# Optimization experiments

Hardware: AMD Instinct MI355X
Metric: run time of the kernel (lower is better)

Reference implementation:

```python
import jax, jax.numpy as jnp
import numpy as np
from jax import lax

V, H, B, S, N, E = 32000, 128, 8, 512, 50000, 600000


def lstm(x, W_ih, W_hh, b):
    # x: [B,T,D]; W_ih: [4H,D]; W_hh: [4H,H]; b: [4H] (b_ih+b_hh combined)
    Bsz = x.shape[0]
    Hd = W_hh.shape[1]
    xg = jnp.einsum('btd,gd->btg', x, W_ih) + b  # precompute input gates [B,T,4H]
    h0 = jnp.zeros((Bsz, Hd), x.dtype)
    c0 = jnp.zeros((Bsz, Hd), x.dtype)

    def step(carry, g_t):
        h, c = carry
        g = g_t + h @ W_hh.T
        i, f, gg, o = jnp.split(g, 4, axis=-1)
        i = jax.nn.sigmoid(i)
        f = jax.nn.sigmoid(f)
        gg = jnp.tanh(gg)
        o = jax.nn.sigmoid(o)
        c = f * c + i * gg
        h = o * jnp.tanh(c)
        return (h, c), h

    _, hs = lax.scan(step, (h0, c0), jnp.swapaxes(xg, 0, 1))
    return jnp.swapaxes(hs, 0, 1)  # [B,T,H]


def gcn_conv(x, W, b, src, dst, n_nodes):
    # PyG GCNConv: add self-loops, symmetric normalization, out = A_hat (x W) + b
    h = x @ W.T  # [N,H]
    deg = jax.ops.segment_sum(jnp.ones(src.shape[0], x.dtype), dst, num_segments=n_nodes) + 1.0
    dinv = lax.rsqrt(deg)
    norm = dinv[src] * dinv[dst]  # [E]
    agg = jax.ops.segment_sum(h[src] * norm[:, None], dst, num_segments=n_nodes)
    agg = agg + h * (dinv * dinv)[:, None]  # self-loop contribution
    return agg + b


def setup_inputs() -> dict:
    key = jax.random.key(0)
    ks = jax.random.split(key, 20)
    s = 0.02
    return {
        'json_input': jax.random.randint(ks[0], (B, S), 0, V, dtype=jnp.int32),
        'node_ids': jax.random.randint(ks[1], (N,), 0, V, dtype=jnp.int32),
        'edge_index': jax.random.randint(ks[2], (2, E), 0, N, dtype=jnp.int32),
        'embedding': jax.random.normal(ks[3], (V, H), jnp.float32) * s,
        'W_ih_enc': jax.random.normal(ks[4], (4 * H, H), jnp.float32) * s,
        'W_hh_enc': jax.random.normal(ks[5], (4 * H, H), jnp.float32) * s,
        'b_enc': jnp.zeros((4 * H,), jnp.float32),
        'W1': jax.random.normal(ks[6], (H, H), jnp.float32) * s,
        'b1': jnp.zeros((H,), jnp.float32),
        'W2': jax.random.normal(ks[7], (H, H), jnp.float32) * s,
        'b2': jnp.zeros((H,), jnp.float32),
        'Wf': jax.random.normal(ks[8], (H, 2 * H), jnp.float32) * s,
        'bf': jnp.zeros((H,), jnp.float32),
        'W_ih_dec': jax.random.normal(ks[9], (4 * H, H), jnp.float32) * s,
        'W_hh_dec': jax.random.normal(ks[10], (4 * H, H), jnp.float32) * s,
        'b_dec': jnp.zeros((4 * H,), jnp.float32),
        'Wo': jax.random.normal(ks[11], (V, H), jnp.float32) * s,
        'bo': jnp.zeros((V,), jnp.float32),
    }


def reference(json_input, node_ids, edge_index, embedding, W_ih_enc, W_hh_enc, b_enc,
              W1, b1, W2, b2, Wf, bf, W_ih_dec, W_hh_dec, b_dec, Wo, bo):
    src, dst = edge_index[0], edge_index[1]
    # sequence branch
    json_emb = embedding[json_input]                      # [B,S,H]
    json_encoded = lstm(json_emb, W_ih_enc, W_hh_enc, b_enc)  # [B,S,H]
    # graph branch
    node_x = embedding[node_ids]                          # [N,H]
    x = gcn_conv(node_x, W1, b1, src, dst, node_ids.shape[0])
    x = gcn_conv(x, W2, b2, src, dst, node_ids.shape[0])
    # fusion
    graph_summary = jnp.broadcast_to(x.mean(axis=0, keepdims=True), (json_encoded.shape[0], x.shape[1]))
    combined = jnp.concatenate([json_encoded.mean(axis=1), graph_summary], axis=1)  # [B,2H]
    fused = combined @ Wf.T + bf                          # [B,H]
    fused_seq = jnp.broadcast_to(fused[:, None, :], (fused.shape[0], json_input.shape[1], fused.shape[1]))
    # decode
    decoded = lstm(fused_seq, W_ih_dec, W_hh_dec, b_dec)  # [B,S,H]
    return decoded @ Wo.T + bo                            # [B,S,V]
```

## Files before the change

### kernel.cpp

```cpp
#include <hip/hip_runtime.h>
#include <hip/hip_bf16.h>
#include <stdint.h>

#define VV 32000
#define HH 128
#define BB 8
#define SS 512
#define NNODE 50000
#define NEDGE 600000
#define NWORK 240

typedef __attribute__((ext_vector_type(8))) short s16x8;
typedef __attribute__((ext_vector_type(4))) float f32x4;

__device__ __forceinline__ void workers_barrier(int* bar, int tid) {
  __syncthreads();
  if (tid == 0) {
    int g = __hip_atomic_load(&bar[32], __ATOMIC_ACQUIRE, __HIP_MEMORY_SCOPE_AGENT);
    int old = __hip_atomic_fetch_add(&bar[0], 1, __ATOMIC_ACQ_REL, __HIP_MEMORY_SCOPE_AGENT);
    if (old == NWORK-1) {
      __hip_atomic_store(&bar[0], 0, __ATOMIC_RELAXED, __HIP_MEMORY_SCOPE_AGENT);
      __hip_atomic_store(&bar[32], g+1, __ATOMIC_RELEASE, __HIP_MEMORY_SCOPE_AGENT);
    } else {
      while (__hip_atomic_load(&bar[32], __ATOMIC_ACQUIRE, __HIP_MEMORY_SCOPE_AGENT) == g)
        __builtin_amdgcn_s_sleep(32);
    }
  }
  __syncthreads();
}

__global__ __launch_bounds__(512) void front_kernel(
    const int* __restrict__ jin, const float* __restrict__ emb,
    const float* __restrict__ WihE, const float* __restrict__ bE,
    float* xg, const float* __restrict__ WhhE, float* __restrict__ hmean,
    const float* __restrict__ Wo, __hip_bfloat16* __restrict__ Bhi, __hip_bfloat16* __restrict__ Blo,
    const int* __restrict__ esrc, const int* __restrict__ edst, const int* __restrict__ nids,
    float* __restrict__ deg, float* __restrict__ dinv, float* __restrict__ s1,
    float* __restrict__ s2, float* __restrict__ cc, float* __restrict__ ee,
    float* __restrict__ csum, float* __restrict__ gvec,
    const float* __restrict__ W1, const float* __restrict__ b1,
    const float* __restrict__ W2, const float* __restrict__ b2, float* __restrict__ mvec,
    int* ucnt, int* bar)
{
  __shared__ __align__(16) char shraw[131072];
  const int bid = blockIdx.x, tid = threadIdx.x;

  if (bid < 8) {
    float* h_s   = (float*)shraw;
    float* act_s = ((float*)shraw) + 128;
    const int b = bid;

    const f32x4* Wrow = (const f32x4*)(WhhE + (size_t)tid*HH);
    f32x4 w[32];
    #pragma unroll
    for (int k=0;k<32;k++) w[k] = Wrow[k];
    #pragma unroll
    for (int k=0;k<32;k++) asm volatile("" : "+v"(w[k]));

    const float* xgrow = xg + (size_t)b*SS*512;
    if (tid == 0) {
      while (__hip_atomic_load(&ucnt[(b*8+0)*32], __ATOMIC_ACQUIRE, __HIP_MEMORY_SCOPE_AGENT) < 8)
        __builtin_amdgcn_s_sleep(16);
    }
    __syncthreads();
    float xv = xgrow[tid];
    if (tid < 128) h_s[tid] = 0.f;
    float cstate = 0.f, hsum = 0.f;
    __syncthreads();

    for (int t=0;t<SS;t++) {
      if ((t & 63) == 0) {
        int cn = (t >> 6) + 1; if (cn > 7) cn = 7;
        if (tid == 0) {
          while (__hip_atomic_load(&ucnt[(b*8+cn)*32], __ATOMIC_ACQUIRE, __HIP_MEMORY_SCOPE_AGENT) < 8)
            __builtin_amdgcn_s_sleep(16);
        }
        __syncthreads();
      }
      int tn = (t < SS-1) ? (t+1) : t;
      float nxv = xgrow[(size_t)tn*512 + tid];
      float a0=0.f,a1=0.f,a2=0.f,a3=0.f;
      #pragma unroll
      for (int k=0;k<32;k++) {
        f32x4 hv = *(const f32x4*)&h_s[k*4];
        a0 += w[k].x*hv.x; a1 += w[k].y*hv.y;
        a2 += w[k].z*hv.z; a3 += w[k].w*hv.w;
      }
      float s = (a0+a1)+(a2+a3) + xv;
      int gid = tid >> 7;
      float act = (gid==2) ? tanhf(s) : 1.0f/(1.0f+expf(-s));
      act_s[tid] = act;
      __syncthreads();
      if (tid < 128) {
        float i_ = act_s[tid], f_ = act_s[128+tid], g_ = act_s[256+tid], o_ = act_s[384+tid];
        cstate = f_*cstate + i_*g_;
        float hh = o_*tanhf(cstate);
        h_s[tid] = hh;
        hsum += hh;
      }
      xv = nxv;
      __syncthreads();
    }
    if (tid < 128) hmean[b*HH + tid] = hsum * (1.0f/512.0f);
  } else {
    const int wbid = bid - 8;
    float (*arow)[128] = (float(*)[128])shraw;
    float* red = (float*)(shraw + 8*128*4);

    for (int u = wbid; u < 512; u += NWORK) {
      int c = u >> 6, r2 = u & 63, b = r2 >> 3, sub = r2 & 7;
      int row0 = b*512 + c*64 + sub*8;
      if (tid < 256) {
        int r = tid >> 5, c4 = (tid & 31) << 2;
        int tok = jin[row0 + r];
        *(float4*)&arow[r][c4] = *(const float4*)&emb[(size_t)tok*HH + c4];
      }
      __syncthreads();
      const float* w0 = WihE + (size_t)tid*HH;
      float acc[8];
      #pragma unroll
      for (int r=0;r<8;r++) acc[r] = 0.f;
      for (int k=0;k<HH;k+=4) {
        float4 wa = *(const float4*)&w0[k];
        #pragma unroll
        for (int r=0;r<8;r++) {
          float4 av = *(const float4*)&arow[r][k];
          acc[r] += av.x*wa.x + av.y*wa.y + av.z*wa.z + av.w*wa.w;
        }
      }
      float bb = bE[tid];
      #pragma unroll
      for (int r=0;r<8;r++)
        xg[(size_t)(row0+r)*512 + tid] = acc[r] + bb;
      __threadfence();
      __syncthreads();
      if (tid == 0)
        __hip_atomic_fetch_add(&ucnt[(b*8+c)*32], 1, __ATOMIC_RELEASE, __HIP_MEMORY_SCOPE_AGENT);
      __syncthreads();
    }
    for (int i = wbid*512 + tid; i < VV*HH/4; i += NWORK*512) {
      float4 v = *(const float4*)&Wo[i*4];
      float vv[4] = {v.x, v.y, v.z, v.w};
      #pragma unroll
      for (int k=0;k<4;k++) {
        __hip_bfloat16 h = __float2bfloat16(vv[k]);
        Bhi[i*4+k] = h;
        Blo[i*4+k] = __float2bfloat16(vv[k] - __bfloat162float(h));
      }
    }
    workers_barrier(bar, tid);
    for (int i = wbid*512 + tid; i < NEDGE; i += NWORK*512)
      atomicAdd(&deg[edst[i]], 1.0f);
    workers_barrier(bar, tid);
    for (int n = wbid*512 + tid; n < NNODE; n += NWORK*512)
      dinv[n] = 1.0f / sqrtf(deg[n] + 1.0f);
    workers_barrier(bar, tid);
    for (int i = wbid*512 + tid; i < NEDGE; i += NWORK*512)
      atomicAdd(&s1[esrc[i]], dinv[edst[i]]);
    workers_barrier(bar, tid);
    {
      float lsum = 0.f;
      for (int n = wbid*512 + tid; n < NNODE; n += NWORK*512) {
        float d = dinv[n]; float v = d*s1[n] + d*d; cc[n] = v; lsum += v;
      }
      red[tid] = lsum; __syncthreads();
      for (int sfl=256; sfl>0; sfl>>=1) { if (tid < sfl) red[tid] += red[tid+sfl]; __syncthreads(); }
      if (tid==0) atomicAdd(csum, red[0]);
    }
    workers_barrier(bar, tid);
    for (int i = wbid*512 + tid; i < NEDGE; i += NWORK*512) {
      int d = edst[i]; atomicAdd(&s2[esrc[i]], cc[d]*dinv[d]);
    }
    workers_barrier(bar, tid);
    for (int n = wbid*512 + tid; n < NNODE; n += NWORK*512) {
      float d = dinv[n]; ee[n] = d*s2[n] + cc[n]*d*d;
    }
    workers_barrier(bar, tid);
    {
      int j = tid & 127, sub = tid >> 7;
      float acc = 0.f;
      for (int n = wbid*4 + sub; n < NNODE; n += NWORK*4)
        acc += ee[n] * emb[(size_t)nids[n]*HH + j];
      red[tid] = acc; __syncthreads();
      if (tid < 128) atomicAdd(&gvec[j], red[tid] + red[tid+128] + red[tid+256] + red[tid+384]);
    }
    workers_barrier(bar, tid);
    if (wbid == 0 && tid < 128) {
      float* gs = (float*)shraw;
      float* v1 = gs + 128;
      int j = tid;
      gs[j] = gvec[j];
      __builtin_amdgcn_s_barrier();
      float a = 0.f;
      for (int k=0;k<128;k++) a += gs[k]*W1[j*128+k];
      v1[j] = a + csum[0]*b1[j];
      __builtin_amdgcn_s_barrier();
      float a2 = 0.f;
      for (int k=0;k<128;k++) a2 += v1[k]*W2[j*128+k];
      mvec[j] = a2 * (1.0f/(float)NNODE) + b2[j];
    }
  }
}

__global__ __launch_bounds__(512) void dec_gemm_kernel(
    const float* __restrict__ xgdec, const float* __restrict__ Whh,
    __hip_bfloat16* __restrict__ ahi, __hip_bfloat16* __restrict__ alo,
    const __hip_bfloat16* __restrict__ Bhi, const __hip_bfloat16* __restrict__ Blo,
    const float* __restrict__ bo, float* __restrict__ out, int* __restrict__ prog)
{
  __shared__ __align__(16) char shraw[131072];
  const int bid = blockIdx.x, tid = threadIdx.x;

  if (bid < 8) {
    float* h_s   = (float*)shraw;
    float* act_s = ((float*)shraw) + 128;
    const int b = bid;

    const f32x4* Wrow = (const f32x4*)(Whh + (size_t)tid*HH);
    f32x4 w[32];
    #pragma unroll
    for (int k=0;k<32;k++) w[k] = Wrow[k];
    #pragma unroll
    for (int k=0;k<32;k++) asm volatile("" : "+v"(w[k]));

    float xv = xgdec[b*512 + tid];
    if (tid < 128) h_s[tid] = 0.f;
    float cstate = 0.f;
    __syncthreads();

    for (int t=0;t<SS;t++) {
      float a0=0.f,a1=0.f,a2=0.f,a3=0.f;
      #pragma unroll
      for (int k=0;k<32;k++) {
        f32x4 hv = *(const f32x4*)&h_s[k*4];
        a0 += w[k].x*hv.x; a1 += w[k].y*hv.y;
        a2 += w[k].z*hv.z; a3 += w[k].w*hv.w;
      }
      float s = (a0+a1)+(a2+a3) + xv;
      int gid = tid >> 7;
      float act = (gid==2) ? tanhf(s) : 1.0f/(1.0f+expf(-s));
      act_s[tid] = act;
      __syncthreads();
      if (tid < 128) {
        float i_ = act_s[tid], f_ = act_s[128+tid], g_ = act_s[256+tid], o_ = act_s[384+tid];
        cstate = f_*cstate + i_*g_;
        float hh = o_*tanhf(cstate);
        h_s[tid] = hh;
        size_t row = (size_t)b*SS + t;
        __hip_bfloat16 hi = __float2bfloat16(hh);
        float rem = hh - __bfloat162float(hi);
        ahi[row*HH + tid] = hi;
        alo[row*HH + tid] = __float2bfloat16(rem);
      }
      __syncthreads();
      if ((t & 63) == 63) {
        __threadfence();
        __syncthreads();
        if (tid == 0)
          __hip_atomic_store(&prog[b*32], (t >> 6) + 1,
                             __ATOMIC_RELEASE, __HIP_MEMORY_SCOPE_AGENT);
      }
    }
  } else {
    short* smem = (short*)shraw;
    const int gbid = bid - 8;
    const int c    = gbid / 1000;
    const int r    = gbid % 1000;
    const int b    = r / 125;
    const int nblk = r % 125;
    const int mbase0 = b*512 + c*64;

    if (tid == 0) {
      while (__hip_atomic_load(&prog[b*32], __ATOMIC_ACQUIRE,
                               __HIP_MEMORY_SCOPE_AGENT) <= c)
        __builtin_amdgcn_s_sleep(64);
    }
    __syncthreads();

    const short* bsrc[2] = {
      (const short*)Bhi + (size_t)nblk*256*HH,
      (const short*)Blo + (size_t)nblk*256*HH };
    #pragma unroll
    for (int p=0;p<2;p++) {
      #pragma unroll
      for (int it=0; it<8; it++) {
        int off  = it*8192 + tid*16;
        int row  = off >> 8;
        int soff = off ^ ((row & 15) << 4);
        __builtin_amdgcn_global_load_lds(
          (const __attribute__((address_space(1))) void*)((const char*)bsrc[p] + soff),
          (__attribute__((address_space(3))) void*)((char*)smem + p*65536 + off),
          16, 0, 0);
      }
    }
    __syncthreads();

    const int lane = tid & 63;
    const int wid  = tid >> 6;
    const int wm = wid >> 2, wn = wid & 3;
    const int l15 = lane & 15, l4 = lane >> 4;
    const int mbase = mbase0 + wm*32;
    const short* Ah = (const short*)ahi;
    const short* Al = (const short*)alo;

    f32x4 acc[2][4] = {};
    #pragma unroll
    for (int s=0;s<4;s++) {
      s16x8 bh[4], bl[4], ah[2], al[2];
      #pragma unroll
      for (int qn=0;qn<4;qn++) {
        int rb   = wn*64 + qn*16 + l15;
        int offb = (rb*256 + s*64 + l4*16) ^ ((rb & 15) << 4);
        bh[qn] = *(const s16x8*)((const char*)smem + offb);
        bl[qn] = *(const s16x8*)((const char*)smem + 65536 + offb);
      }
      #pragma unroll
      for (int qm=0;qm<2;qm++) {
        int arow = mbase + qm*16 + l15;
        size_t aoff = (size_t)arow*HH + s*32 + l4*8;
        ah[qm] = *(const s16x8*)(Ah + aoff);
        al[qm] = *(const s16x8*)(Al + aoff);
      }
      #pragma unroll
      for (int qm=0;qm<2;qm++) {
        #pragma unroll
        for (int qn=0;qn<4;qn++) {
          acc[qm][qn] = __builtin_amdgcn_mfma_f32_16x16x32_bf16(bh[qn], ah[qm], acc[qm][qn], 0,0,0);
          acc[qm][qn] = __builtin_amdgcn_mfma_f32_16x16x32_bf16(bl[qn], ah[qm], acc[qm][qn], 0,0,0);
          acc[qm][qn] = __builtin_amdgcn_mfma_f32_16x16x32_bf16(bh[qn], al[qm], acc[qm][qn], 0,0,0);
        }
      }
    }
    #pragma unroll
    for (int qm=0;qm<2;qm++) {
      int row = mbase + qm*16 + l15;
      #pragma unroll
      for (int qn=0;qn<4;qn++) {
        int colb = nblk*256 + wn*64 + qn*16 + l4*4;
        f32x4 bv = *(const f32x4*)&bo[colb];
        f32x4 o = acc[qm][qn] + bv;
        *(f32x4*)&out[(size_t)row*VV + colb] = o;
      }
    }
  }
}

__global__ __launch_bounds__(512) void fusion_kernel(const float* __restrict__ hmean, const float* __restrict__ mvec,
    const float* __restrict__ Wf, const float* __restrict__ bfv,
    const float* __restrict__ Wihd, const float* __restrict__ bd, float* __restrict__ xgdec)
{
  __shared__ float comb[256];
  __shared__ float fus[128];
  int b = blockIdx.x, tid = threadIdx.x;
  if (tid < 128) comb[tid] = hmean[b*128 + tid];
  else if (tid < 256) comb[tid] = mvec[tid - 128];
  __syncthreads();
  if (tid < 128) {
    float a = 0.f;
    for (int k=0;k<256;k++) a += comb[k]*Wf[tid*256+k];
    fus[tid] = a + bfv[tid];
  }
  __syncthreads();
  float a = 0.f;
  for (int k=0;k<128;k++) a += fus[k]*Wihd[tid*128+k];
  xgdec[b*512 + tid] = a + bd[tid];
}

extern "C" void kernel_launch(void* const* d_in, const int* in_sizes, int n_in,
                              void* d_out, int out_size, void* d_ws, size_t ws_size,
                              hipStream_t stream)
{
  (void)in_sizes; (void)n_in; (void)out_size; (void)ws_size;
  const int*   jin   = (const int*)d_in[0];
  const int*   nids  = (const int*)d_in[1];
  const int*   esrc  = (const int*)d_in[2];
  const int*   edst  = esrc + NEDGE;
  const float* emb   = (const float*)d_in[3];
  const float* WihE  = (const float*)d_in[4];
  const float* WhhE  = (const float*)d_in[5];
  const float* bE    = (const float*)d_in[6];
  const float* W1    = (const float*)d_in[7];
  const float* b1    = (const float*)d_in[8];
  const float* W2    = (const float*)d_in[9];
  const float* b2    = (const float*)d_in[10];
  const float* Wf    = (const float*)d_in[11];
  const float* bfv   = (const float*)d_in[12];
  const float* WihD  = (const float*)d_in[13];
  const float* WhhD  = (const float*)d_in[14];
  const float* bD    = (const float*)d_in[15];
  const float* Wo    = (const float*)d_in[16];
  const float* bo    = (const float*)d_in[17];
  float* out = (float*)d_out;

  char* ws = (char*)d_ws;
  size_t off = 0;
  auto alloc = [&](size_t bytes) { size_t o = off; off = (off + bytes + 255) & ~(size_t)255; return o; };

  int*   prog = (int*)(ws + alloc(BB*32*4));
  int*   ucnt = (int*)(ws + alloc(BB*8*32*4));
  int*   bar  = (int*)(ws + alloc(64*4));
  float* deg  = (float*)(ws + alloc(NNODE*4));
  float* s1   = (float*)(ws + alloc(NNODE*4));
  float* s2   = (float*)(ws + alloc(NNODE*4));
  float* gvec = (float*)(ws + alloc(128*4));
  float* csum = (float*)(ws + alloc(4));
  size_t zero_bytes = off;
  float* dinv = (float*)(ws + alloc(NNODE*4));
  float* cc   = (float*)(ws + alloc(NNODE*4));
  float* ee   = (float*)(ws + alloc(NNODE*4));
  float* mvec = (float*)(ws + alloc(128*4));
  float* hmean= (float*)(ws + alloc(BB*HH*4));
  float* xgdec= (float*)(ws + alloc(BB*512*4));
  float* xgenc= (float*)(ws + alloc((size_t)BB*SS*512*4));
  __hip_bfloat16* Ahi = (__hip_bfloat16*)(ws + alloc((size_t)BB*SS*HH*2));
  __hip_bfloat16* Alo = (__hip_bfloat16*)(ws + alloc((size_t)BB*SS*HH*2));
  __hip_bfloat16* Bhi = (__hip_bfloat16*)(ws + alloc((size_t)VV*HH*2));
  __hip_bfloat16* Blo = (__hip_bfloat16*)(ws + alloc((size_t)VV*HH*2));

  hipMemsetAsync(ws, 0, zero_bytes, stream);

  front_kernel<<<dim3(8 + NWORK), dim3(512), 0, stream>>>(
      jin, emb, WihE, bE, xgenc, WhhE, hmean, Wo, Bhi, Blo,
      esrc, edst, nids, deg, dinv, s1, s2, cc, ee, csum, gvec,
      W1, b1, W2, b2, mvec, ucnt, bar);

  fusion_kernel<<<dim3(BB), dim3(512), 0, stream>>>(hmean, mvec, Wf, bfv, WihD, bD, xgdec);
  dec_gemm_kernel<<<dim3(8 + 8000), dim3(512), 0, stream>>>(
      xgdec, WhhD, Ahi, Alo, Bhi, Blo, bo, out, prog);
}
```

Baseline: 1.252 ms.

## Split encoder input GEMM into own kernel and use persistent decoder GEMM blocks

Result: faster. 1.176 ms (-6.1%).

```diff
diff --git a/kernel.cpp b/kernel.cpp
--- a/kernel.cpp
+++ b/kernel.cpp
@@ -29,18 +29,55 @@
   __syncthreads();
 }
 
+__global__ __launch_bounds__(256) void xg_enc_kernel(
+    const int* __restrict__ jin, const float* __restrict__ emb,
+    const float* __restrict__ Wih, const float* __restrict__ bvec,
+    float* __restrict__ xg)
+{
+  __shared__ __align__(16) float arow[8][128];
+  const int tid = threadIdx.x, blk = blockIdx.x;
+  {
+    int r = tid >> 5, c = (tid & 31) << 2;
+    int tok = jin[blk*8 + r];
+    *(float4*)&arow[r][c] = *(const float4*)&emb[(size_t)tok*HH + c];
+  }
+  __syncthreads();
+  const int g0 = tid * 2;
+  const float* w0 = Wih + (size_t)g0*HH;
+  const float* w1 = w0 + HH;
+  float acc0[8], acc1[8];
+  #pragma unroll
+  for (int r=0;r<8;r++){ acc0[r]=0.f; acc1[r]=0.f; }
+  for (int k=0;k<HH;k+=4) {
+    float4 wa = *(const float4*)&w0[k];
+    float4 wb = *(const float4*)&w1[k];
+    #pragma unroll
+    for (int r=0;r<8;r++) {
+      float4 av = *(const float4*)&arow[r][k];
+      acc0[r] += av.x*wa.x + av.y*wa.y + av.z*wa.z + av.w*wa.w;
+      acc1[r] += av.x*wb.x + av.y*wb.y + av.z*wb.z + av.w*wb.w;
+    }
+  }
+  float bb0 = bvec[g0], bb1 = bvec[g0+1];
+  #pragma unroll
+  for (int r=0;r<8;r++) {
+    size_t row = (size_t)blk*8 + r;
+    xg[row*512 + g0]     = acc0[r] + bb0;
+    xg[row*512 + g0 + 1] = acc1[r] + bb1;
+  }
+}
+
 __global__ __launch_bounds__(512) void front_kernel(
-    const int* __restrict__ jin, const float* __restrict__ emb,
-    const float* __restrict__ WihE, const float* __restrict__ bE,
-    float* xg, const float* __restrict__ WhhE, float* __restrict__ hmean,
+    const float* __restrict__ xg, const float* __restrict__ WhhE, float* __restrict__ hmean,
     const float* __restrict__ Wo, __hip_bfloat16* __restrict__ Bhi, __hip_bfloat16* __restrict__ Blo,
     const int* __restrict__ esrc, const int* __restrict__ edst, const int* __restrict__ nids,
+    const float* __restrict__ emb,
     float* __restrict__ deg, float* __restrict__ dinv, float* __restrict__ s1,
     float* __restrict__ s2, float* __restrict__ cc, float* __restrict__ ee,
     float* __restrict__ csum, float* __restrict__ gvec,
     const float* __restrict__ W1, const float* __restrict__ b1,
     const float* __restrict__ W2, const float* __restrict__ b2, float* __restrict__ mvec,
-    int* ucnt, int* bar)
+    int* bar)
 {
   __shared__ __align__(16) char shraw[131072];
   const int bid = blockIdx.x, tid = threadIdx.x;
@@ -58,25 +95,12 @@
     for (int k=0;k<32;k++) asm volatile("" : "+v"(w[k]));
 
     const float* xgrow = xg + (size_t)b*SS*512;
-    if (tid == 0) {
-      while (__hip_atomic_load(&ucnt[(b*8+0)*32], __ATOMIC_ACQUIRE, __HIP_MEMORY_SCOPE_AGENT) < 8)
-        __builtin_amdgcn_s_sleep(16);
-    }
-    __syncthreads();
     float xv = xgrow[tid];
     if (tid < 128) h_s[tid] = 0.f;
     float cstate = 0.f, hsum = 0.f;
     __syncthreads();
 
     for (int t=0;t<SS;t++) {
-      if ((t & 63) == 0) {
-        int cn = (t >> 6) + 1; if (cn > 7) cn = 7;
-        if (tid == 0) {
-          while (__hip_atomic_load(&ucnt[(b*8+cn)*32], __ATOMIC_ACQUIRE, __HIP_MEMORY_SCOPE_AGENT) < 8)
-            __builtin_amdgcn_s_sleep(16);
-        }
-        __syncthreads();
-      }
       int tn = (t < SS-1) ? (t+1) : t;
       float nxv = xgrow[(size_t)tn*512 + tid];
       float a0=0.f,a1=0.f,a2=0.f,a3=0.f;
@@ -104,40 +128,8 @@
     if (tid < 128) hmean[b*HH + tid] = hsum * (1.0f/512.0f);
   } else {
     const int wbid = bid - 8;
-    float (*arow)[128] = (float(*)[128])shraw;
-    float* red = (float*)(shraw + 8*128*4);
-
-    for (int u = wbid; u < 512; u += NWORK) {
-      int c = u >> 6, r2 = u & 63, b = r2 >> 3, sub = r2 & 7;
-      int row0 = b*512 + c*64 + sub*8;
-      if (tid < 256) {
-        int r = tid >> 5, c4 = (tid & 31) << 2;
-        int tok = jin[row0 + r];
-        *(float4*)&arow[r][c4] = *(const float4*)&emb[(size_t)tok*HH + c4];
-      }
-      __syncthreads();
-      const float* w0 = WihE + (size_t)tid*HH;
-      float acc[8];
-      #pragma unroll
-      for (int r=0;r<8;r++) acc[r] = 0.f;
-      for (int k=0;k<HH;k+=4) {
-        float4 wa = *(const float4*)&w0[k];
-        #pragma unroll
-        for (int r=0;r<8;r++) {
-          float4 av = *(const float4*)&arow[r][k];
-          acc[r] += av.x*wa.x + av.y*wa.y + av.z*wa.z + av.w*wa.w;
-        }
-      }
-      float bb = bE[tid];
-      #pragma unroll
-      for (int r=0;r<8;r++)
-        xg[(size_t)(row0+r)*512 + tid] = acc[r] + bb;
-      __threadfence();
-      __syncthreads();
-      if (tid == 0)
-        __hip_atomic_fetch_add(&ucnt[(b*8+c)*32], 1, __ATOMIC_RELEASE, __HIP_MEMORY_SCOPE_AGENT);
-      __syncthreads();
-    }
+    float* red = (float*)shraw;
+
     for (int i = wbid*512 + tid; i < VV*HH/4; i += NWORK*512) {
       float4 v = *(const float4*)&Wo[i*4];
       float vv[4] = {v.x, v.y, v.z, v.w};
@@ -185,19 +177,22 @@
       if (tid < 128) atomicAdd(&gvec[j], red[tid] + red[tid+128] + red[tid+256] + red[tid+384]);
     }
     workers_barrier(bar, tid);
-    if (wbid == 0 && tid < 128) {
+    if (wbid == 0) {
       float* gs = (float*)shraw;
       float* v1 = gs + 128;
-      int j = tid;
-      gs[j] = gvec[j];
-      __builtin_amdgcn_s_barrier();
-      float a = 0.f;
-      for (int k=0;k<128;k++) a += gs[k]*W1[j*128+k];
-      v1[j] = a + csum[0]*b1[j];
-      __builtin_amdgcn_s_barrier();
-      float a2 = 0.f;
-      for (int k=0;k<128;k++) a2 += v1[k]*W2[j*128+k];
-      mvec[j] = a2 * (1.0f/(float)NNODE) + b2[j];
+      if (tid < 128) gs[tid] = gvec[tid];
+      __syncthreads();
+      if (tid < 128) {
+        float a = 0.f;
+        for (int k=0;k<128;k++) a += gs[k]*W1[tid*128+k];
+        v1[tid] = a + csum[0]*b1[tid];
+      }
+      __syncthreads();
+      if (tid < 128) {
+        float a2 = 0.f;
+        for (int k=0;k<128;k++) a2 += v1[k]*W2[tid*128+k];
+        mvec[tid] = a2 * (1.0f/(float)NNODE) + b2[tid];
+      }
     }
   }
 }
@@ -263,19 +258,10 @@
     }
   } else {
     short* smem = (short*)shraw;
-    const int gbid = bid - 8;
-    const int c    = gbid / 1000;
-    const int r    = gbid % 1000;
-    const int b    = r / 125;
-    const int nblk = r % 125;
-    const int mbase0 = b*512 + c*64;
-
-    if (tid == 0) {
-      while (__hip_atomic_load(&prog[b*32], __ATOMIC_ACQUIRE,
-                               __HIP_MEMORY_SCOPE_AGENT) <= c)
-        __builtin_amdgcn_s_sleep(64);
-    }
-    __syncthreads();
+    const int o = bid - 8;
+    int nblk, b0, nb;
+    if (o < 230) { nblk = o >> 1; b0 = (o & 1) * 4; nb = 4; }
+    else         { nblk = 115 + (o - 230); b0 = 0; nb = 8; }
 
     const short* bsrc[2] = {
       (const short*)Bhi + (size_t)nblk*256*HH,
@@ -299,47 +285,59 @@
     const int wid  = tid >> 6;
     const int wm = wid >> 2, wn = wid & 3;
     const int l15 = lane & 15, l4 = lane >> 4;
-    const int mbase = mbase0 + wm*32;
     const short* Ah = (const short*)ahi;
     const short* Al = (const short*)alo;
 
-    f32x4 acc[2][4] = {};
-    #pragma unroll
-    for (int s=0;s<4;s++) {
-      s16x8 bh[4], bl[4], ah[2], al[2];
-      #pragma unroll
-      for (int qn=0;qn<4;qn++) {
-        int rb   = wn*64 + qn*16 + l15;
-        int offb = (rb*256 + s*64 + l4*16) ^ ((rb & 15) << 4);
-        bh[qn] = *(const s16x8*)((const char*)smem + offb);
-        bl[qn] = *(const s16x8*)((const char*)smem + 65536 + offb);
-      }
-      #pragma unroll
-      for (int qm=0;qm<2;qm++) {
-        int arow = mbase + qm*16 + l15;
-        size_t aoff = (size_t)arow*HH + s*32 + l4*8;
-        ah[qm] = *(const s16x8*)(Ah + aoff);
-        al[qm] = *(const s16x8*)(Al + aoff);
-      }
-      #pragma unroll
-      for (int qm=0;qm<2;qm++) {
+    for (int c = 0; c < 8; ++c) {
+      for (int bi = 0; bi < nb; ++bi) {
+        int b = b0 + bi;
+        if (tid == 0) {
+          while (__hip_atomic_load(&prog[b*32], __ATOMIC_ACQUIRE,
+                                   __HIP_MEMORY_SCOPE_AGENT) <= c)
+            __builtin_amdgcn_s_sleep(64);
+        }
+        __syncthreads();
+
+        const int mbase = b*512 + c*64 + wm*32;
+        f32x4 acc[2][4] = {};
         #pragma unroll
-        for (int qn=0;qn<4;qn++) {
-          acc[qm][qn] = __builtin_amdgcn_mfma_f32_16x16x32_bf16(bh[qn], ah[qm], acc[qm][qn], 0,0,0);
-          acc[qm][qn] = __builtin_amdgcn_mfma_f32_16x16x32_bf16(bl[qn], ah[qm], acc[qm][qn], 0,0,0);
-          acc[qm][qn] = __builtin_amdgcn_mfma_f32_16x16x32_bf16(bh[qn], al[qm], acc[qm][qn], 0,0,0);
+        for (int s=0;s<4;s++) {
+          s16x8 bh[4], bl[4], ah[2], al[2];
+          #pragma unroll
+          for (int qn=0;qn<4;qn++) {
+            int rb   = wn*64 + qn*16 + l15;
+            int offb = (rb*256 + s*64 + l4*16) ^ ((rb & 15) << 4);
+            bh[qn] = *(const s16x8*)((const char*)smem + offb);
+            bl[qn] = *(const s16x8*)((const char*)smem + 65536 + offb);
+          }
+          #pragma unroll
+          for (int qm=0;qm<2;qm++) {
+            int arow = mbase + qm*16 + l15;
+            size_t aoff = (size_t)arow*HH + s*32 + l4*8;
+            ah[qm] = *(const s16x8*)(Ah + aoff);
+            al[qm] = *(const s16x8*)(Al + aoff);
+          }
+          #pragma unroll
+          for (int qm=0;qm<2;qm++) {
+            #pragma unroll
+            for (int qn=0;qn<4;qn++) {
+              acc[qm][qn] = __builtin_amdgcn_mfma_f32_16x16x32_bf16(bh[qn], ah[qm], acc[qm][qn], 0,0,0);
+              acc[qm][qn] = __builtin_amdgcn_mfma_f32_16x16x32_bf16(bl[qn], ah[qm], acc[qm][qn], 0,0,0);
+              acc[qm][qn] = __builtin_amdgcn_mfma_f32_16x16x32_bf16(bh[qn], al[qm], acc[qm][qn], 0,0,0);
+            }
+          }
         }
-      }
-    }
-    #pragma unroll
-    for (int qm=0;qm<2;qm++) {
-      int row = mbase + qm*16 + l15;
-      #pragma unroll
-      for (int qn=0;qn<4;qn++) {
-        int colb = nblk*256 + wn*64 + qn*16 + l4*4;
-        f32x4 bv = *(const f32x4*)&bo[colb];
-        f32x4 o = acc[qm][qn] + bv;
-        *(f32x4*)&out[(size_t)row*VV + colb] = o;
+        #pragma unroll
+        for (int qm=0;qm<2;qm++) {
+          int row = mbase + qm*16 + l15;
+          #pragma unroll
+          for (int qn=0;qn<4;qn++) {
+            int colb = nblk*256 + wn*64 + qn*16 + l4*4;
+            f32x4 bv = *(const f32x4*)&bo[colb];
+            f32x4 oo = acc[qm][qn] + bv;
+            *(f32x4*)&out[(size_t)row*VV + colb] = oo;
+          }
+        }
       }
     }
   }
@@ -397,7 +395,6 @@
   auto alloc = [&](size_t bytes) { size_t o = off; off = (off + bytes + 255) & ~(size_t)255; return o; };
 
   int*   prog = (int*)(ws + alloc(BB*32*4));
-  int*   ucnt = (int*)(ws + alloc(BB*8*32*4));
   int*   bar  = (int*)(ws + alloc(64*4));
   float* deg  = (float*)(ws + alloc(NNODE*4));
   float* s1   = (float*)(ws + alloc(NNODE*4));
@@ -419,12 +416,14 @@
 
   hipMemsetAsync(ws, 0, zero_bytes, stream);
 
+  xg_enc_kernel<<<dim3((BB*SS)/8), dim3(256), 0, stream>>>(jin, emb, WihE, bE, xgenc);
+
   front_kernel<<<dim3(8 + NWORK), dim3(512), 0, stream>>>(
-      jin, emb, WihE, bE, xgenc, WhhE, hmean, Wo, Bhi, Blo,
-      esrc, edst, nids, deg, dinv, s1, s2, cc, ee, csum, gvec,
-      W1, b1, W2, b2, mvec, ucnt, bar);
+      xgenc, WhhE, hmean, Wo, Bhi, Blo,
+      esrc, edst, nids, emb, deg, dinv, s1, s2, cc, ee, csum, gvec,
+      W1, b1, W2, b2, mvec, bar);
 
   fusion_kernel<<<dim3(BB), dim3(512), 0, stream>>>(hmean, mvec, Wf, bfv, WihD, bD, xgdec);
-  dec_gemm_kernel<<<dim3(8 + 8000), dim3(512), 0, stream>>>(
+  dec_gemm_kernel<<<dim3(8 + NWORK), dim3(512), 0, stream>>>(
       xgdec, WhhD, Ahi, Alo, Bhi, Blo, bo, out, prog);
 }
```
